# Kernel optimization log

Hardware: AMD Instinct MI355X
Metric: run time of the kernel (lower is better)

The kernel has to match this reference:

```python
import jax, jax.numpy as jnp
import numpy as np

B, N_FRAMES, C, S = 4, 32, 256, 16
D = 512            # attn_dim = min(C*S*S, 512)
NHEADS = 8
TOKEN = C * S * S  # 65536
EPS = 1e-5


def _layer_norm_last(x, g, b):
    mu = x.mean(-1, keepdims=True)
    var = x.var(-1, keepdims=True)
    return (x - mu) * jax.lax.rsqrt(var + EPS) * g + b


def _forward(feat, Wp, bp, Wu, bu, Wq, bq, Wk, bk, Wv, bv, Wo, bo, ln1_g, ln1_b,
             Wk1, bk1, Wk2, bk2, Wpc, bpc, gn_g, gn_b, Wf1, bf1, Wf2, bf2,
             dn_g, dn_b, num_frames):
    BN, Cc, H, W = feat.shape
    N = num_frames
    Bb = BN // N
    # 1) flatten frames to tokens and project (B, N, token_dim) -> (B, N, D)
    tokens = feat.reshape(Bb, N, Cc * H * W)
    tp = tokens @ Wp.T + bp
    # contextual grouping with clamped indices: K = v_{n-1}, Q = v_n, V = v_{n+1}
    idx = jnp.arange(N)
    v_prev = tp[:, jnp.maximum(idx - 1, 0)]
    v_next = tp[:, jnp.minimum(idx + 1, N - 1)]
    # 2) MHA with seq_len 1 for Q/K/V (degenerate softmax over a single key)
    dh = D // NHEADS
    q = (tp @ Wq.T + bq).reshape(Bb, N, NHEADS, dh)
    k = (v_prev @ Wk.T + bk).reshape(Bb, N, NHEADS, dh)
    v = (v_next @ Wv.T + bv).reshape(Bb, N, NHEADS, dh)
    scores = jnp.sum(q * k, axis=-1, keepdims=True) / jnp.sqrt(jnp.float32(dh))  # (B,N,h,1)
    wts = jax.nn.softmax(scores, axis=-1)  # identically 1.0 (single key)
    attn = (wts * v).reshape(Bb, N, D) @ Wo.T + bo
    enh = _layer_norm_last(attn + tp, ln1_g, ln1_b)
    # 3) unproject back to feature maps
    feat_attn = (enh @ Wu.T + bu).reshape(BN, Cc, H, W)
    # 4) DynamicConv: per-sample depthwise 3x3 kernels conditioned on GAP
    gap = feat_attn.mean((2, 3))                       # (BN, C)
    hid = jax.nn.relu(gap @ Wk1.T + bk1)
    kern = (hid @ Wk2.T + bk2).reshape(BN, Cc, 3, 3)   # per-sample, per-channel kernels
    xp = jnp.pad(feat_attn, ((0, 0), (0, 0), (1, 1), (1, 1)))
    out = jnp.zeros_like(feat_attn)
    for di in range(3):  # fixed 3x3 kernel taps
        for dj in range(3):
            out = out + kern[:, :, di, dj][:, :, None, None] * xp[:, :, di:di + H, dj:dj + W]
    # 1x1 proj conv
    out = jnp.einsum('nchw,dc->ndhw', out, Wpc) + bpc[:, None, None]
    # GroupNorm(min(32,C))
    G = min(32, Cc)
    og = out.reshape(BN, G, -1)
    mu = og.mean(-1, keepdims=True)
    var = og.var(-1, keepdims=True)
    out = ((og - mu) * jax.lax.rsqrt(var + EPS)).reshape(BN, Cc, H, W)
    feat_dc = out * gn_g[:, None, None] + gn_b[:, None, None]
    # 5) dc_fc (1x1 conv -> relu -> 1x1 conv) + residual, then LayerNorm([C,S,S])
    y = jax.nn.relu(jnp.einsum('nchw,dc->ndhw', feat_dc, Wf1) + bf1[:, None, None])
    y = jnp.einsum('nchw,dc->ndhw', y, Wf2) + bf2[:, None, None]
    z = y + feat_attn
    zf = z.reshape(BN, -1)
    mu = zf.mean(-1, keepdims=True)
    var = zf.var(-1, keepdims=True)
    zn = ((zf - mu) * jax.lax.rsqrt(var + EPS)).reshape(BN, Cc, H, W)
    return zn * dn_g + dn_b


def setup_inputs() -> dict:
    key = jax.random.key(0)
    ks = jax.random.split(key, 16)
    sc = 0.02
    inp = {
        'feat': jax.random.normal(ks[0], (B * N_FRAMES, C, S, S), jnp.float32),
        'Wp': jax.random.normal(ks[1], (D, TOKEN), jnp.float32) * sc,
        'bp': jnp.zeros((D,), jnp.float32),
        'Wu': jax.random.normal(ks[2], (TOKEN, D), jnp.float32) * sc,
        'bu': jnp.zeros((TOKEN,), jnp.float32),
        'Wq': jax.random.normal(ks[3], (D, D), jnp.float32) * sc,
        'bq': jnp.zeros((D,), jnp.float32),
        'Wk': jax.random.normal(ks[4], (D, D), jnp.float32) * sc,
        'bk': jnp.zeros((D,), jnp.float32),
        'Wv': jax.random.normal(ks[5], (D, D), jnp.float32) * sc,
        'bv': jnp.zeros((D,), jnp.float32),
        'Wo': jax.random.normal(ks[6], (D, D), jnp.float32) * sc,
        'bo': jnp.zeros((D,), jnp.float32),
        'ln1_g': jnp.ones((D,), jnp.float32),
        'ln1_b': jnp.zeros((D,), jnp.float32),
        'Wk1': jax.random.normal(ks[7], (C, C), jnp.float32) * sc,
        'bk1': jnp.zeros((C,), jnp.float32),
        'Wk2': jax.random.normal(ks[8], (C * 9, C), jnp.float32) * sc,
        'bk2': jnp.zeros((C * 9,), jnp.float32),
        'Wpc': jax.random.normal(ks[9], (C, C), jnp.float32) * sc,
        'bpc': jnp.zeros((C,), jnp.float32),
        'gn_g': jnp.ones((C,), jnp.float32),
        'gn_b': jnp.zeros((C,), jnp.float32),
        'Wf1': jax.random.normal(ks[10], (C, C), jnp.float32) * sc,
        'bf1': jnp.zeros((C,), jnp.float32),
        'Wf2': jax.random.normal(ks[11], (C, C), jnp.float32) * sc,
        'bf2': jnp.zeros((C,), jnp.float32),
        'dn_g': jnp.ones((C, S, S), jnp.float32),
        'dn_b': jnp.zeros((C, S, S), jnp.float32),
        'num_frames': N_FRAMES,
    }
    return inp


def reference(feat, Wp, bp, Wu, bu, Wq, bq, Wk, bk, Wv, bv, Wo, bo, ln1_g, ln1_b,
              Wk1, bk1, Wk2, bk2, Wpc, bpc, gn_g, gn_b, Wf1, bf1, Wf2, bf2,
              dn_g, dn_b, num_frames):
    return _forward(feat, Wp, bp, Wu, bu, Wq, bq, Wk, bk, Wv, bv, Wo, bo,
                    ln1_g, ln1_b, Wk1, bk1, Wk2, bk2, Wpc, bpc, gn_g, gn_b,
                    Wf1, bf1, Wf2, bf2, dn_g, dn_b, num_frames)
```

## Files before the change

### kernel.cpp

```cpp
#include <hip/hip_runtime.h>


typedef unsigned short u16;
typedef unsigned int u32;
typedef __attribute__((ext_vector_type(8))) short short8;
typedef __attribute__((ext_vector_type(4))) float floatx4;

__device__ __forceinline__ float b2f(u16 h){ return __uint_as_float(((u32)h)<<16); }
__device__ __forceinline__ u16 f2b(float f){
  u32 u = __float_as_uint(f);
  u = (u + 0x7FFFu + ((u>>16)&1u)) >> 16;
  return (u16)u;
}
__device__ __forceinline__ float blo(u32 w){ return __uint_as_float(w<<16); }
__device__ __forceinline__ float bhi(u32 w){ return __uint_as_float(w & 0xFFFF0000u); }
__device__ __forceinline__ bool probe_f32(const u32* p){ return p[0]==0x3F800000u; }

__device__ __forceinline__ float wred(float v){
  #pragma unroll
  for (int o=32;o>0;o>>=1) v += __shfl_down(v, o, 64);
  return v;
}

__device__ __forceinline__ float dot8(uint4 u, const float* t){
  return t[0]*blo(u.x)+t[1]*bhi(u.x)+t[2]*blo(u.y)+t[3]*bhi(u.y)
       + t[4]*blo(u.z)+t[5]*bhi(u.z)+t[6]*blo(u.w)+t[7]*bhi(u.w);
}

__device__ __forceinline__ void bar_lgkm(){
  asm volatile("s_waitcnt lgkmcnt(0)" ::: "memory");
  __builtin_amdgcn_sched_barrier(0);
  __builtin_amdgcn_s_barrier();
  asm volatile("" ::: "memory");
}
__device__ __forceinline__ void bar(){
  asm volatile("" ::: "memory");
  __builtin_amdgcn_s_barrier();
  asm volatile("" ::: "memory");
}

struct SrcTab { const void* p[22]; };

__global__ __launch_bounds__(256) void cvt_k(SrcTab st, const u32* probe, u16* dst){
  constexpr int ns[22]   = {262144,262144,65536,589824,65536,65536,65536,65536,65536,
                            65536,512,512,512,512,512,256,2304,256,256,256,256,256};
  constexpr int offs[22] = {0,262144,524288,589824,1179648,1245184,1310720,1376256,1441792,
                            1507328,1572864,1573376,1573888,1574400,1574912,1575424,1575680,
                            1577984,1578240,1578496,1578752,1579008};
  int t = blockIdx.y;
  int e = (blockIdx.x*256 + threadIdx.x)*4;
  if (e >= ns[t]) return;
  u16* d = dst + offs[t] + e;
  if (probe_f32(probe)){
    float4 v = *(const float4*)((const float*)st.p[t] + e);
    d[0]=f2b(v.x); d[1]=f2b(v.y); d[2]=f2b(v.z); d[3]=f2b(v.w);
  } else {
    *(uint2*)d = *(const uint2*)((const u16*)st.p[t] + e);
  }
}

template<int MODE>
__global__ __launch_bounds__(256) void gemm_k(
    const void* __restrict__ Ap, int lda,
    const void* __restrict__ Bp, int ldb,
    void* __restrict__ Cp, int N, int Ktot, int kchunk,
    const u16* __restrict__ bias,
    const float* __restrict__ gnst,
    const u16* __restrict__ gng, const u16* __restrict__ gnb,
    const u16* __restrict__ fres,
    const u32* __restrict__ probe, int araw, int braw)
{
  __shared__ __align__(16) u16 As[64*72];
  __shared__ __align__(16) u16 Bs[64*72];

  const bool pf32 = probe_f32(probe);
  const bool a32 = araw && pf32, b32 = braw && pf32;

  const int tid = threadIdx.x;
  const int lane = tid & 63, wv = tid >> 6;
  const int mw = wv >> 1, nw = wv & 1;
  const int m0 = blockIdx.x * 64, n0 = blockIdx.y * 64;
  int k0 = 0, kend = Ktot;
  if (MODE == 0) { k0 = blockIdx.z * kchunk; kend = k0 + kchunk; }

  floatx4 zf = {0.f,0.f,0.f,0.f};
  floatx4 acc[2][2];
  acc[0][0]=zf; acc[0][1]=zf; acc[1][0]=zf; acc[1][1]=zf;

  const int ml = lane & 15, q = lane >> 4;
  const int ar0 = (mw*32 + ml)*72 + q*8;
  const int ar1 = ar0 + 16*72;
  const int br0 = (nw*32 + ml)*72 + q*8;
  const int br1 = br0 + 16*72;

  const int row0 = tid >> 3, colc = tid & 7;

  auto ld_tiles = [&](uint4 (&pa)[2][2], uint4 (&pb)[2][2], int kk){
    #pragma unroll
    for (int i=0;i<2;i++){
      int row = row0 + i*32;
      if (a32){
        const float* s = (const float*)Ap + (size_t)(m0+row)*lda + kk + colc*8;
        pa[i][0] = ((const uint4*)s)[0];
        pa[i][1] = ((const uint4*)s)[1];
      } else {
        const u16* s = (const u16*)Ap + (size_t)(m0+row)*lda + kk + colc*8;
        pa[i][0] = *(const uint4*)s;
      }
      if (b32){
        const float* s = (const float*)Bp + (size_t)(n0+row)*ldb + kk + colc*8;
        pb[i][0] = ((const uint4*)s)[0];
        pb[i][1] = ((const uint4*)s)[1];
      } else {
        const u16* s = (const u16*)Bp + (size_t)(n0+row)*ldb + kk + colc*8;
        pb[i][0] = *(const uint4*)s;
      }
    }
  };

  auto stage = [&](uint4 (&pa)[2][2], uint4 (&pb)[2][2], int kk){
    #pragma unroll
    for (int i=0;i<2;i++){
      int row = row0 + i*32;
      u16* adst = &As[row*72 + colc*8];
      if (MODE == 3){
        uint4 u = pa[i][0];
        int nsamp = (m0+row) >> 8;
        int cbase = kk + colc*8;
        int g = cbase >> 3;
        float mu = gnst[(nsamp*32+g)*2], rs = gnst[(nsamp*32+g)*2+1];
        float f[8] = {blo(u.x),bhi(u.x),blo(u.y),bhi(u.y),blo(u.z),bhi(u.z),blo(u.w),bhi(u.w)};
        u16 tmp[8];
        #pragma unroll
        for (int j=0;j<8;j++){
          int c = cbase + j;
          tmp[j] = f2b((f[j]-mu)*rs*b2f(gng[c]) + b2f(gnb[c]));
        }
        *(uint4*)adst = *(uint4*)tmp;
      } else if (a32){
        uint4 v0 = pa[i][0], v1 = pa[i][1];
        u16 tmp[8];
        tmp[0]=f2b(__uint_as_float(v0.x)); tmp[1]=f2b(__uint_as_float(v0.y));
        tmp[2]=f2b(__uint_as_float(v0.z)); tmp[3]=f2b(__uint_as_float(v0.w));
        tmp[4]=f2b(__uint_as_float(v1.x)); tmp[5]=f2b(__uint_as_float(v1.y));
        tmp[6]=f2b(__uint_as_float(v1.z)); tmp[7]=f2b(__uint_as_float(v1.w));
        *(uint4*)adst = *(uint4*)tmp;
      } else {
        *(uint4*)adst = pa[i][0];
      }
      u16* bdst = &Bs[row*72 + colc*8];
      if (b32){
        uint4 v0 = pb[i][0], v1 = pb[i][1];
        u16 tmp[8];
        tmp[0]=f2b(__uint_as_float(v0.x)); tmp[1]=f2b(__uint_as_float(v0.y));
        tmp[2]=f2b(__uint_as_float(v0.z)); tmp[3]=f2b(__uint_as_float(v0.w));
        tmp[4]=f2b(__uint_as_float(v1.x)); tmp[5]=f2b(__uint_as_float(v1.y));
        tmp[6]=f2b(__uint_as_float(v1.z)); tmp[7]=f2b(__uint_as_float(v1.w));
        *(uint4*)bdst = *(uint4*)tmp;
      } else {
        *(uint4*)bdst = pb[i][0];
      }
    }
  };

  auto mfma_step = [&](){
    #pragma unroll
    for (int ks2=0; ks2<2; ks2++){
      int ko = ks2*32;
      short8 a0 = *(const short8*)&As[ar0 + ko];
      short8 a1 = *(const short8*)&As[ar1 + ko];
      short8 b0 = *(const short8*)&Bs[br0 + ko];
      short8 b1 = *(const short8*)&Bs[br1 + ko];
      acc[0][0] = __builtin_amdgcn_mfma_f32_16x16x32_bf16(a0, b0, acc[0][0], 0,0,0);
      acc[0][1] = __builtin_amdgcn_mfma_f32_16x16x32_bf16(a0, b1, acc[0][1], 0,0,0);
      acc[1][0] = __builtin_amdgcn_mfma_f32_16x16x32_bf16(a1, b0, acc[1][0], 0,0,0);
      acc[1][1] = __builtin_amdgcn_mfma_f32_16x16x32_bf16(a1, b1, acc[1][1], 0,0,0);
    }
  };

  uint4 pa0[2][2], pb0[2][2], pa1[2][2], pb1[2][2];
  ld_tiles(pa0, pb0, k0);
  for (int kk = k0; kk < kend; kk += 128){
    bar();
    ld_tiles(pa1, pb1, kk + 64);
    stage(pa0, pb0, kk);
    bar_lgkm();
    mfma_step();
    bar();
    if (kk + 128 < kend) ld_tiles(pa0, pb0, kk + 128);
    stage(pa1, pb1, kk + 64);
    bar_lgkm();
    mfma_step();
  }

  const int colg = lane & 15, quad = lane >> 4;
  #pragma unroll
  for (int mi=0;mi<2;mi++){
    #pragma unroll
    for (int ni=0;ni<2;ni++){
      #pragma unroll
      for (int r=0;r<4;r++){
        int m = m0 + mw*32 + mi*16 + quad*4 + r;
        int n = n0 + nw*32 + ni*16 + colg;
        float v = acc[mi][ni][r];
        if (MODE==0){
          atomicAdd(&((float*)Cp)[(size_t)m*N + n], v);
        } else if (MODE==1){
          ((u16*)Cp)[(size_t)m*N + n] = f2b(v + b2f(bias[n]));
        } else if (MODE==3){
          ((u16*)Cp)[(size_t)m*N + n] = f2b(fmaxf(v + b2f(bias[n]), 0.f));
        } else if (MODE==4){
          int nsp = m >> 8, s = m & 255;
          ((u16*)Cp)[(size_t)m*N + n] =
              f2b(v + b2f(bias[n]) + b2f(fres[(size_t)nsp*65536 + (size_t)n*256 + s]));
        }
      }
    }
  }
}

__global__ __launch_bounds__(512) void attn_ln_k(
    const float* __restrict__ tp, const u16* __restrict__ Wv, const u16* __restrict__ bv,
    const u16* __restrict__ Wo, const u16* __restrict__ bo, const u16* __restrict__ bp,
    const u16* __restrict__ g, const u16* __restrict__ bln, u16* __restrict__ enh)
{
  __shared__ float tpr[512], tpn[512], vv[512], red[16];
  int r = blockIdx.x; int n = r & 31; int rn = (n==31) ? r : r+1;
  int t = threadIdx.x;
  float bpv = b2f(bp[t]);
  tpr[t] = tp[(size_t)r*512 + t] + bpv;
  tpn[t] = tp[(size_t)rn*512 + t] + bpv;
  __syncthreads();
  {
    const uint4* w4 = (const uint4*)(Wv + (size_t)t*512);
    float acc = b2f(bv[t]);
    #pragma unroll 8
    for (int i=0;i<64;i++) acc += dot8(w4[i], &tpn[i*8]);
    vv[t] = acc;
  }
  __syncthreads();
  float x;
  {
    const uint4* w4 = (const uint4*)(Wo + (size_t)t*512);
    float acc = b2f(bo[t]);
    #pragma unroll 8
    for (int i=0;i<64;i++) acc += dot8(w4[i], &vv[i*8]);
    x = acc + tpr[t];
  }
  float s1 = wred(x), s2 = wred(x*x);
  int lane = t & 63, wid = t >> 6;
  if (lane==0){ red[wid] = s1; red[8+wid] = s2; }
  __syncthreads();
  if (t==0){
    float a=0.f, b=0.f;
    #pragma unroll
    for (int i=0;i<8;i++){ a += red[i]; b += red[8+i]; }
    float mu = a/512.f; float var = b/512.f - mu*mu;
    red[0]=mu; red[1]=rsqrtf(var+1e-5f);
  }
  __syncthreads();
  float mu = red[0], rs = red[1];
  enh[(size_t)r*512 + t] = f2b((x-mu)*rs*b2f(g[t]) + b2f(bln[t]));
}

__global__ __launch_bounds__(256) void gap_k(const u16* __restrict__ fa, float* __restrict__ gapb){
  int wid = threadIdx.x>>6, lane = threadIdx.x&63;
  int pair = blockIdx.x*4 + wid;
  const uint2* p = (const uint2*)(fa + (size_t)pair*256);
  uint2 v = p[lane];
  float s = wred(blo(v.x)+bhi(v.x)+blo(v.y)+bhi(v.y));
  if (lane==0) gapb[pair] = s * (1.0f/256.0f);
}

__global__ __launch_bounds__(256) void hidkern_k(
    const float* __restrict__ gapb, const u16* __restrict__ Wk1, const u16* __restrict__ bk1,
    const u16* __restrict__ Wk2, const u16* __restrict__ bk2, float* __restrict__ kernb)
{
  __shared__ float gl[256], hl[256];
  int nn = blockIdx.x, t = threadIdx.x;
  gl[t] = gapb[(size_t)nn*256 + t];
  __syncthreads();
  {
    const uint4* w4 = (const uint4*)(Wk1 + (size_t)t*256);
    float acc = b2f(bk1[t]);
    #pragma unroll 8
    for (int i=0;i<32;i++) acc += dot8(w4[i], &gl[i*8]);
    hl[t] = fmaxf(acc, 0.f);
  }
  __syncthreads();
  for (int qq=0; qq<9; qq++){
    int e = t*9 + qq;
    const uint4* w4 = (const uint4*)(Wk2 + (size_t)e*256);
    float acc = b2f(bk2[e]);
    #pragma unroll 8
    for (int i=0;i<32;i++) acc += dot8(w4[i], &hl[i*8]);
    kernb[(size_t)nn*2304 + e] = acc;
  }
}

__global__ __launch_bounds__(256) void conv_k(
    const u16* __restrict__ fa, const float* __restrict__ kernb, u16* __restrict__ dwb)
{
  int b = blockIdx.x; int h = b & 15; int nn = b >> 4; int c = threadIdx.x;
  float kv[9];
  #pragma unroll
  for (int qq=0; qq<9; qq++) kv[qq] = kernb[(size_t)nn*2304 + c*9 + qq];
  float rowv[3][18];
  #pragma unroll
  for (int di=0; di<3; di++){
    int hh = h + di - 1;
    if (hh >= 0 && hh < 16){
      const u16* rp = fa + (size_t)nn*65536 + (size_t)c*256 + hh*16;
      rowv[di][0] = 0.f; rowv[di][17] = 0.f;
      #pragma unroll
      for (int w=0; w<16; w++) rowv[di][w+1] = b2f(rp[w]);
    } else {
      #pragma unroll
      for (int x=0; x<18; x++) rowv[di][x] = 0.f;
    }
  }
  #pragma unroll
  for (int w=0; w<16; w++){
    float o = 0.f;
    #pragma unroll
    for (int di=0; di<3; di++)
      o += kv[di*3]*rowv[di][w] + kv[di*3+1]*rowv[di][w+1] + kv[di*3+2]*rowv[di][w+2];
    dwb[((size_t)nn*256 + h*16 + w)*256 + c] = f2b(o);
  }
}

__global__ __launch_bounds__(256) void gnstats_k(const u16* __restrict__ out2, float* __restrict__ gnst){
  int wid = threadIdx.x>>6, lane = threadIdx.x&63;
  int grp = blockIdx.x*4 + wid; int nn = grp >> 5; int gg = grp & 31;
  const u16* base = out2 + (size_t)nn*65536 + gg*8;
  float s=0.f, ss=0.f;
  #pragma unroll 4
  for (int i=0;i<32;i++){
    int f = i*64 + lane; int sidx = f >> 3; int j = f & 7;
    float v = b2f(base[(size_t)sidx*256 + j]);
    s += v; ss += v*v;
  }
  s = wred(s); ss = wred(ss);
  if (lane==0){
    float mu = s/2048.f; float var = ss/2048.f - mu*mu;
    gnst[grp*2] = mu; gnst[grp*2+1] = rsqrtf(var + 1e-5f);
  }
}

__global__ __launch_bounds__(256) void lnstats_k(const u16* __restrict__ z, float* __restrict__ lnst){
  __shared__ float red[8];
  int nn = blockIdx.x, t = threadIdx.x;
  const uint4* p = (const uint4*)(z + (size_t)nn*65536);
  float s=0.f, ss=0.f;
  for (int i=0;i<32;i++){
    uint4 v = p[(size_t)i*256 + t];
    float f0=blo(v.x),f1=bhi(v.x),f2=blo(v.y),f3=bhi(v.y);
    float f4=blo(v.z),f5=bhi(v.z),f6=blo(v.w),f7=bhi(v.w);
    s  += (f0+f1)+(f2+f3)+(f4+f5)+(f6+f7);
    ss += (f0*f0+f1*f1)+(f2*f2+f3*f3)+(f4*f4+f5*f5)+(f6*f6+f7*f7);
  }
  s = wred(s); ss = wred(ss);
  int lane = t&63, wid = t>>6;
  if (lane==0){ red[wid]=s; red[4+wid]=ss; }
  __syncthreads();
  if (t==0){
    float a=red[0]+red[1]+red[2]+red[3];
    float b=red[4]+red[5]+red[6]+red[7];
    float mu = a/65536.f; float var = b/65536.f - mu*mu;
    lnst[nn*2] = mu; lnst[nn*2+1] = rsqrtf(var + 1e-5f);
  }
}

__global__ __launch_bounds__(256) void final_k(
    const u16* __restrict__ z, const float* __restrict__ lnst,
    const u16* __restrict__ dng, const u16* __restrict__ dnb,
    void* __restrict__ outp, const u32* __restrict__ probe)
{
  __shared__ float zt[32*257];
  const bool pf32 = probe_f32(probe);
  int b = blockIdx.x; int nn = b >> 3; int s0 = (b & 7)*32;
  int t = threadIdx.x;
  {
    int srow = t >> 3; int c0 = (t & 7)*32;
    const uint4* p = (const uint4*)(z + (size_t)nn*65536 + (size_t)(s0+srow)*256 + c0);
    float* dst = &zt[srow*257 + c0];
    #pragma unroll
    for (int i=0;i<4;i++){
      uint4 v = p[i];
      dst[i*8+0]=blo(v.x); dst[i*8+1]=bhi(v.x); dst[i*8+2]=blo(v.y); dst[i*8+3]=bhi(v.y);
      dst[i*8+4]=blo(v.z); dst[i*8+5]=bhi(v.z); dst[i*8+6]=blo(v.w); dst[i*8+7]=bhi(v.w);
    }
  }
  __syncthreads();
  float mu = lnst[nn*2], rs = lnst[nn*2+1];
  int sl = t & 31, cq = t >> 5;
  for (int i=0;i<32;i++){
    int c = i*8 + cq;
    float v = (zt[sl*257 + c] - mu) * rs;
    int gidx = c*256 + s0 + sl;
    float res = v*b2f(dng[gidx]) + b2f(dnb[gidx]);
    size_t oi = (size_t)nn*65536 + gidx;
    if (pf32) ((float*)outp)[oi] = res;
    else      ((u16*)outp)[oi]   = f2b(res);
  }
}

extern "C" void kernel_launch(void* const* d_in, const int* in_sizes, int n_in,
                              void* d_out, int out_size, void* d_ws, size_t ws_size,
                              hipStream_t stream) {
  (void)in_sizes; (void)n_in; (void)out_size; (void)ws_size;
  const u32* probe = (const u32*)d_in[21];

  char* w = (char*)d_ws;
  u16* cvt = (u16*)w;
  u16 *cWv  = cvt+0,       *cWo  = cvt+262144, *cWk1 = cvt+524288, *cWk2 = cvt+589824;
  u16 *cWpc = cvt+1179648, *cWf1 = cvt+1245184,*cWf2 = cvt+1310720;
  u16 *cdng = cvt+1376256, *cdnb = cvt+1441792,*cbu  = cvt+1507328;
  u16 *cbp  = cvt+1572864, *cbv  = cvt+1573376,*cbo  = cvt+1573888;
  u16 *cln1g= cvt+1574400, *cln1b= cvt+1574912,*cbk1 = cvt+1575424,*cbk2 = cvt+1575680;
  u16 *cbpc = cvt+1577984, *cgng = cvt+1578240,*cgnb = cvt+1578496;
  u16 *cbf1 = cvt+1578752, *cbf2 = cvt+1579008;

  float* tp_raw = (float*)(w + 4194304);
  u16*   enh    = (u16*)  (w + 4456448);
  float* gapb   = (float*)(w + 4587520);
  float* kernb  = (float*)(w + 4718592);
  float* gnst   = (float*)(w + 5898240);
  float* lnst   = (float*)(w + 5931008);
  u16*   fa     = (u16*)  (w + 8388608);
  u16*   out2   = (u16*)  (w + 25165824);
  u16*   z      = out2;
  u16*   dwb    = (u16*)d_out;
  u16*   y1     = dwb;

  SrcTab st;
  st.p[0]=d_in[9];  st.p[1]=d_in[11]; st.p[2]=d_in[15]; st.p[3]=d_in[17];
  st.p[4]=d_in[19]; st.p[5]=d_in[23]; st.p[6]=d_in[25]; st.p[7]=d_in[27];
  st.p[8]=d_in[28]; st.p[9]=d_in[4];  st.p[10]=d_in[2]; st.p[11]=d_in[10];
  st.p[12]=d_in[12];st.p[13]=d_in[13];st.p[14]=d_in[14];st.p[15]=d_in[16];
  st.p[16]=d_in[18];st.p[17]=d_in[20];st.p[18]=d_in[21];st.p[19]=d_in[22];
  st.p[20]=d_in[24];st.p[21]=d_in[26];

  cvt_k<<<dim3(576,22), 256, 0, stream>>>(st, probe, cvt);
  hipMemsetAsync(tp_raw, 0, 128*512*4, stream);
  gemm_k<0><<<dim3(2,8,128), 256, 0, stream>>>(d_in[0], 65536, d_in[1], 65536, tp_raw,
      512, 65536, 512, nullptr, nullptr, nullptr, nullptr, nullptr, probe, 1, 1);
  attn_ln_k<<<128, 512, 0, stream>>>(tp_raw, cWv, cbv, cWo, cbo, cbp, cln1g, cln1b, enh);
  gemm_k<1><<<dim3(2,1024,1), 256, 0, stream>>>(enh, 512, d_in[3], 512, fa,
      65536, 512, 0, cbu, nullptr, nullptr, nullptr, nullptr, probe, 0, 1);
  gap_k<<<8192, 256, 0, stream>>>(fa, gapb);
  hidkern_k<<<128, 256, 0, stream>>>(gapb, cWk1, cbk1, cWk2, cbk2, kernb);
  conv_k<<<2048, 256, 0, stream>>>(fa, kernb, dwb);
  gemm_k<1><<<dim3(512,4,1), 256, 0, stream>>>(dwb, 256, cWpc, 256, out2,
      256, 256, 0, cbpc, nullptr, nullptr, nullptr, nullptr, probe, 0, 0);
  gnstats_k<<<1024, 256, 0, stream>>>(out2, gnst);
  gemm_k<3><<<dim3(512,4,1), 256, 0, stream>>>(out2, 256, cWf1, 256, y1,
      256, 256, 0, cbf1, gnst, cgng, cgnb, nullptr, probe, 0, 0);
  gemm_k<4><<<dim3(512,4,1), 256, 0, stream>>>(y1, 256, cWf2, 256, z,
      256, 256, 0, cbf2, nullptr, nullptr, nullptr, fa, probe, 0, 0);
  lnstats_k<<<128, 256, 0, stream>>>(z, lnst);
  final_k<<<1024, 256, 0, stream>>>(z, lnst, cdng, cdnb, d_out, probe);
}
```

Baseline: 616.4 us.

## Double-buffer GEMM LDS tiles and use packed bf16 conversion instruction

The GEMM kernel now keeps two LDS tile buffers and alternates between them. This removes the extra barrier that used to precede each staging step, and global loads are issued two k-steps ahead. The scalar software fp32-to-bf16 rounding in the staging path is replaced by the v_cvt_pk_bf16_f32 instruction, which converts two values at once. The cost is double the LDS footprint and more registers held live for prefetched tiles, which may reduce occupancy.

```diff
diff --git a/kernel.cpp b/kernel.cpp
--- a/kernel.cpp
+++ b/kernel.cpp
@@ -12,6 +12,11 @@
   u = (u + 0x7FFFu + ((u>>16)&1u)) >> 16;
   return (u16)u;
 }
+__device__ __forceinline__ u32 cvtpk(float lo, float hi){
+  u32 r;
+  asm("v_cvt_pk_bf16_f32 %0, %1, %2" : "=v"(r) : "v"(lo), "v"(hi));
+  return r;
+}
 __device__ __forceinline__ float blo(u32 w){ return __uint_as_float(w<<16); }
 __device__ __forceinline__ float bhi(u32 w){ return __uint_as_float(w & 0xFFFF0000u); }
 __device__ __forceinline__ bool probe_f32(const u32* p){ return p[0]==0x3F800000u; }
@@ -30,11 +35,6 @@
 __device__ __forceinline__ void bar_lgkm(){
   asm volatile("s_waitcnt lgkmcnt(0)" ::: "memory");
   __builtin_amdgcn_sched_barrier(0);
-  __builtin_amdgcn_s_barrier();
-  asm volatile("" ::: "memory");
-}
-__device__ __forceinline__ void bar(){
-  asm volatile("" ::: "memory");
   __builtin_amdgcn_s_barrier();
   asm volatile("" ::: "memory");
 }
@@ -70,8 +70,10 @@
     const u16* __restrict__ fres,
     const u32* __restrict__ probe, int araw, int braw)
 {
-  __shared__ __align__(16) u16 As[64*72];
-  __shared__ __align__(16) u16 Bs[64*72];
+  __shared__ __align__(16) u16 As0[64*72];
+  __shared__ __align__(16) u16 Bs0[64*72];
+  __shared__ __align__(16) u16 As1[64*72];
+  __shared__ __align__(16) u16 Bs1[64*72];
 
   const bool pf32 = probe_f32(probe);
   const bool a32 = araw && pf32, b32 = braw && pf32;
@@ -118,7 +120,7 @@
     }
   };
 
-  auto stage = [&](uint4 (&pa)[2][2], uint4 (&pb)[2][2], int kk){
+  auto stage = [&](uint4 (&pa)[2][2], uint4 (&pb)[2][2], int kk, u16* As, u16* Bs){
     #pragma unroll
     for (int i=0;i<2;i++){
       int row = row0 + i*32;
@@ -130,40 +132,43 @@
         int g = cbase >> 3;
         float mu = gnst[(nsamp*32+g)*2], rs = gnst[(nsamp*32+g)*2+1];
         float f[8] = {blo(u.x),bhi(u.x),blo(u.y),bhi(u.y),blo(u.z),bhi(u.z),blo(u.w),bhi(u.w)};
-        u16 tmp[8];
+        float fn[8];
         #pragma unroll
         for (int j=0;j<8;j++){
           int c = cbase + j;
-          tmp[j] = f2b((f[j]-mu)*rs*b2f(gng[c]) + b2f(gnb[c]));
+          fn[j] = (f[j]-mu)*rs*b2f(gng[c]) + b2f(gnb[c]);
         }
-        *(uint4*)adst = *(uint4*)tmp;
+        uint4 t4;
+        t4.x = cvtpk(fn[0],fn[1]); t4.y = cvtpk(fn[2],fn[3]);
+        t4.z = cvtpk(fn[4],fn[5]); t4.w = cvtpk(fn[6],fn[7]);
+        *(uint4*)adst = t4;
       } else if (a32){
         uint4 v0 = pa[i][0], v1 = pa[i][1];
-        u16 tmp[8];
-        tmp[0]=f2b(__uint_as_float(v0.x)); tmp[1]=f2b(__uint_as_float(v0.y));
-        tmp[2]=f2b(__uint_as_float(v0.z)); tmp[3]=f2b(__uint_as_float(v0.w));
-        tmp[4]=f2b(__uint_as_float(v1.x)); tmp[5]=f2b(__uint_as_float(v1.y));
-        tmp[6]=f2b(__uint_as_float(v1.z)); tmp[7]=f2b(__uint_as_float(v1.w));
-        *(uint4*)adst = *(uint4*)tmp;
+        uint4 t4;
+        t4.x = cvtpk(__uint_as_float(v0.x), __uint_as_float(v0.y));
+        t4.y = cvtpk(__uint_as_float(v0.z), __uint_as_float(v0.w));
+        t4.z = cvtpk(__uint_as_float(v1.x), __uint_as_float(v1.y));
+        t4.w = cvtpk(__uint_as_float(v1.z), __uint_as_float(v1.w));
+        *(uint4*)adst = t4;
       } else {
         *(uint4*)adst = pa[i][0];
       }
       u16* bdst = &Bs[row*72 + colc*8];
       if (b32){
         uint4 v0 = pb[i][0], v1 = pb[i][1];
-        u16 tmp[8];
-        tmp[0]=f2b(__uint_as_float(v0.x)); tmp[1]=f2b(__uint_as_float(v0.y));
-        tmp[2]=f2b(__uint_as_float(v0.z)); tmp[3]=f2b(__uint_as_float(v0.w));
-        tmp[4]=f2b(__uint_as_float(v1.x)); tmp[5]=f2b(__uint_as_float(v1.y));
-        tmp[6]=f2b(__uint_as_float(v1.z)); tmp[7]=f2b(__uint_as_float(v1.w));
-        *(uint4*)bdst = *(uint4*)tmp;
+        uint4 t4;
+        t4.x = cvtpk(__uint_as_float(v0.x), __uint_as_float(v0.y));
+        t4.y = cvtpk(__uint_as_float(v0.z), __uint_as_float(v0.w));
+        t4.z = cvtpk(__uint_as_float(v1.x), __uint_as_float(v1.y));
+        t4.w = cvtpk(__uint_as_float(v1.z), __uint_as_float(v1.w));
+        *(uint4*)bdst = t4;
       } else {
         *(uint4*)bdst = pb[i][0];
       }
     }
   };
 
-  auto mfma_step = [&](){
+  auto mfma_step = [&](const u16* As, const u16* Bs){
     #pragma unroll
     for (int ks2=0; ks2<2; ks2++){
       int ko = ks2*32;
@@ -180,17 +185,16 @@
 
   uint4 pa0[2][2], pb0[2][2], pa1[2][2], pb1[2][2];
   ld_tiles(pa0, pb0, k0);
+  ld_tiles(pa1, pb1, k0 + 64);
   for (int kk = k0; kk < kend; kk += 128){
-    bar();
-    ld_tiles(pa1, pb1, kk + 64);
-    stage(pa0, pb0, kk);
+    stage(pa0, pb0, kk, As0, Bs0);
+    if (kk + 128 < kend) ld_tiles(pa0, pb0, kk + 128);
     bar_lgkm();
-    mfma_step();
-    bar();
-    if (kk + 128 < kend) ld_tiles(pa0, pb0, kk + 128);
-    stage(pa1, pb1, kk + 64);
+    mfma_step(As0, Bs0);
+    stage(pa1, pb1, kk + 64, As1, Bs1);
+    if (kk + 192 < kend) ld_tiles(pa1, pb1, kk + 192);
     bar_lgkm();
-    mfma_step();
+    mfma_step(As1, Bs1);
   }
 
   const int colg = lane & 15, quad = lane >> 4;
```

New measurement: 630.7 us. 2.3% more time.
